# Performance work log

Hardware: AMD Instinct MI355X
Metric: run time of the kernel (lower is better)

The kernel has to match this reference:

```python
import jax, jax.numpy as jnp
import numpy as np

B, TOKEN_DIM, HIDDEN_DIM, K = 32768, 1024, 512, 8192


def setup_inputs() -> dict:
    key = jax.random.key(0)
    k1, k2, k3 = jax.random.split(key, 3)
    tokens = jax.random.normal(k1, (B, TOKEN_DIM), dtype=jnp.float32)
    # nn.Linear weight init in the module: randn * 0.1, bias zero
    W = jax.random.normal(k2, (HIDDEN_DIM, TOKEN_DIM), dtype=jnp.float32) * 0.1
    b = jnp.zeros((HIDDEN_DIM,), dtype=jnp.float32)
    codebook = jax.random.normal(k3, (K, HIDDEN_DIM), dtype=jnp.float32)
    return {"tokens": tokens, "W": W, "b": b, "codebook": codebook}


def reference(tokens, W, b, codebook):
    # 1. Linear projection: [B, token_dim] -> [B, hidden_dim]
    h = tokens @ W.T + b
    # 2. Pairwise Euclidean distances to codebook: [B, K]
    #    ||h - c||^2 = ||h||^2 + ||c||^2 - 2 h.c  (clamped for numerical safety)
    h_sq = jnp.sum(h * h, axis=-1, keepdims=True)            # [B, 1]
    c_sq = jnp.sum(codebook * codebook, axis=-1)              # [K]
    d2 = h_sq + c_sq[None, :] - 2.0 * (h @ codebook.T)        # [B, K]
    dist = jnp.sqrt(jnp.maximum(d2, 0.0))
    # 3. Hard nearest-codebook lookup
    return jnp.argmin(dist, axis=-1).astype(jnp.int64)
```

## Files before the change

kernel.cpp:

```cpp
#include <hip/hip_runtime.h>
#include <stdint.h>

typedef __attribute__((ext_vector_type(8))) _Float16 f16x8;
typedef __attribute__((ext_vector_type(4))) float f32x4;

namespace {
constexpr int NB = 32768;
constexpr int TD = 1024;
constexpr int HD = 512;
constexpr int KC = 8192;

constexpr size_t WS_H      = 0;
constexpr size_t WS_CHF    = WS_H + (size_t)NB * HD * 4;
constexpr size_t WS_CSQ32  = WS_CHF + (size_t)KC * HD * 2;
constexpr size_t WS_PART   = WS_CSQ32 + (size_t)KC * 4;
constexpr size_t WS_NEED   = WS_PART + (size_t)NB * 16 * 8;
constexpr size_t WS_H16    = WS_NEED;
constexpr size_t WS_NEED2  = WS_H16 + (size_t)NB * HD * 2;
}

__device__ __forceinline__ void g2lds16(const void* g, void* l) {
    __builtin_amdgcn_global_load_lds(
        (const __attribute__((address_space(1))) void*)g,
        (__attribute__((address_space(3))) void*)l, 16, 0, 0);
}

__global__ void k0_prep_cb(const float* __restrict__ cb, uint8_t* __restrict__ ws) {
    _Float16* chf = (_Float16*)(ws + WS_CHF);
    const int wv = threadIdx.x >> 6, lane = threadIdx.x & 63;
    const int row = blockIdx.x * 4 + wv;
    const size_t base = (size_t)row * HD + lane * 8;
    const float4 a = *(const float4*)&cb[base];
    const float4 b = *(const float4*)&cb[base + 4];
    const float cf[8] = {a.x, a.y, a.z, a.w, b.x, b.y, b.z, b.w};
    f16x8 hv;
    #pragma unroll
    for (int e = 0; e < 8; ++e) hv[e] = (_Float16)cf[e];
    *(f16x8*)&chf[base] = hv;
}

__global__ void k0_csq(const float* __restrict__ cb, uint8_t* __restrict__ ws) {
    float* csq32 = (float*)(ws + WS_CSQ32);
    const int code = blockIdx.x * 256 + threadIdx.x;
    const float* crow = &cb[(size_t)code * HD];
    float sq = 0.0f;
    #pragma unroll 4
    for (int kq = 0; kq < HD / 4; ++kq) {
        const float4 v = *(const float4*)&crow[kq * 4];
        sq = fmaf(v.x, v.x, sq);
        sq = fmaf(v.y, v.y, sq);
        sq = fmaf(v.z, v.z, sq);
        sq = fmaf(v.w, v.w, sq);
    }
    csq32[code] = sq;
}

template<bool H16>
__launch_bounds__(256, 2)
__global__ void k1_hgemm(const float* __restrict__ tokens,
                         const float* __restrict__ W,
                         const float* __restrict__ bias,
                         uint8_t* __restrict__ ws) {
    __shared__ __align__(16) float Tt[32][132];
    __shared__ __align__(16) float Wt[32][132];
    float* h = (float*)(ws + WS_H);
    _Float16* h16 = (_Float16*)(ws + WS_H16);

    const int tid = threadIdx.x;
    const int rows0 = blockIdx.x * 128;
    const int hcol0 = blockIdx.y * 128;
    const int rx = tid & 15;
    const int cx = tid >> 4;
    const int srow = tid >> 1;
    const int shalf = tid & 1;

    float acc[8][8];
    #pragma unroll
    for (int i = 0; i < 8; ++i)
        #pragma unroll
        for (int j = 0; j < 8; ++j) acc[i][j] = 0.0f;

    #pragma unroll 1
    for (int kt = 0; kt < TD; kt += 32) {
        __syncthreads();
        {
            const float* tsrc = &tokens[(size_t)(rows0 + srow) * TD + kt + shalf * 16];
            const float* wsrc = &W[(size_t)(hcol0 + srow) * TD + kt + shalf * 16];
            #pragma unroll
            for (int q = 0; q < 4; ++q) {
                const float4 tv = *(const float4*)&tsrc[q * 4];
                const float4 wv = *(const float4*)&wsrc[q * 4];
                const int k0 = shalf * 16 + q * 4;
                Tt[k0 + 0][srow] = tv.x; Tt[k0 + 1][srow] = tv.y;
                Tt[k0 + 2][srow] = tv.z; Tt[k0 + 3][srow] = tv.w;
                Wt[k0 + 0][srow] = wv.x; Wt[k0 + 1][srow] = wv.y;
                Wt[k0 + 2][srow] = wv.z; Wt[k0 + 3][srow] = wv.w;
            }
        }
        __syncthreads();
        #pragma unroll 2
        for (int kk = 0; kk < 32; ++kk) {
            const float4 a0 = *(const float4*)&Tt[kk][rx * 8];
            const float4 a1 = *(const float4*)&Tt[kk][rx * 8 + 4];
            const float4 b0 = *(const float4*)&Wt[kk][cx * 8];
            const float4 b1 = *(const float4*)&Wt[kk][cx * 8 + 4];
            const float av[8] = {a0.x, a0.y, a0.z, a0.w, a1.x, a1.y, a1.z, a1.w};
            const float bv[8] = {b0.x, b0.y, b0.z, b0.w, b1.x, b1.y, b1.z, b1.w};
            #pragma unroll
            for (int i = 0; i < 8; ++i)
                #pragma unroll
                for (int j = 0; j < 8; ++j)
                    acc[i][j] = fmaf(av[i], bv[j], acc[i][j]);
        }
    }

    float bj[8];
    #pragma unroll
    for (int j = 0; j < 8; ++j) bj[j] = bias[hcol0 + cx * 8 + j];
    #pragma unroll
    for (int i = 0; i < 8; ++i) {
        const int row = rows0 + rx * 8 + i;
        float o[8];
        #pragma unroll
        for (int j = 0; j < 8; ++j) o[j] = acc[i][j] + bj[j];
        float4 o0, o1;
        o0.x = o[0]; o0.y = o[1]; o0.z = o[2]; o0.w = o[3];
        o1.x = o[4]; o1.y = o[5]; o1.z = o[6]; o1.w = o[7];
        *(float4*)&h[(size_t)row * HD + hcol0 + cx * 8] = o0;
        *(float4*)&h[(size_t)row * HD + hcol0 + cx * 8 + 4] = o1;
        if constexpr (H16) {
            f16x8 hv;
            #pragma unroll
            for (int j = 0; j < 8; ++j) hv[j] = (_Float16)o[j];
            *(f16x8*)&h16[(size_t)row * HD + hcol0 + cx * 8] = hv;
        }
    }
}

template<bool H16>
__launch_bounds__(256, 2)
__global__ void k2_score(uint8_t* __restrict__ ws) {
    __shared__ __align__(16) _Float16 At[128 * 32], Bt[128 * 32];
    __shared__ unsigned long long dump[128][16];
    const float* h = (const float*)(ws + WS_H);
    const _Float16* h16 = (const _Float16*)(ws + WS_H16);
    const _Float16* chf = (const _Float16*)(ws + WS_CHF);
    const float* csq32 = (const float*)(ws + WS_CSQ32);
    unsigned long long* part = (unsigned long long*)(ws + WS_PART);

    const int tid = threadIdx.x;
    const int l = tid & 63;
    const int w = tid >> 6;
    const int wr = w >> 1, wc = w & 1;
    const int rows0 = blockIdx.x * 128;
    const int codes0 = blockIdx.y * 2048;

    unsigned long long cand0[16], cand1[16];
    #pragma unroll
    for (int s = 0; s < 16; ++s) { cand0[s] = ~0ull; cand1[s] = ~0ull; }

    #pragma unroll 1
    for (int cc = 0; cc < 16; ++cc) {
        const int codebase = codes0 + cc * 128;
        f32x4 acc[4][4];
        #pragma unroll
        for (int m = 0; m < 4; ++m)
            #pragma unroll
            for (int n = 0; n < 4; ++n) acc[m][n] = (f32x4)(0.0f);

        #pragma unroll 1
        for (int kt = 0; kt < HD; kt += 32) {
            __syncthreads();
            if constexpr (H16) {
                #pragma unroll
                for (int i = 0; i < 2; ++i) {
                    const int sub = w * 2 + i;
                    const int arow = sub * 16 + (l >> 2);
                    g2lds16(h16 + (size_t)(rows0 + arow) * HD + kt + (l & 3) * 8,
                            At + sub * 512);
                    const int crow = sub * 16 + (l >> 2);
                    g2lds16(chf + (size_t)(codebase + crow) * HD + kt + (l & 3) * 8,
                            Bt + sub * 512);
                }
            } else {
                #pragma unroll
                for (int i = 0; i < 2; ++i) {
                    const int sub = w * 2 + i;
                    const int crow = sub * 16 + (l >> 2);
                    g2lds16(chf + (size_t)(codebase + crow) * HD + kt + (l & 3) * 8,
                            Bt + sub * 512);
                }
                const int arow = tid >> 1, ahalf = tid & 1;
                const float* hsrc = &h[(size_t)(rows0 + arow) * HD + kt + ahalf * 16];
                const float4 q0 = *(const float4*)&hsrc[0];
                const float4 q1 = *(const float4*)&hsrc[4];
                const float4 q2 = *(const float4*)&hsrc[8];
                const float4 q3 = *(const float4*)&hsrc[12];
                f16x8 v0, v1;
                v0[0] = (_Float16)q0.x; v0[1] = (_Float16)q0.y;
                v0[2] = (_Float16)q0.z; v0[3] = (_Float16)q0.w;
                v0[4] = (_Float16)q1.x; v0[5] = (_Float16)q1.y;
                v0[6] = (_Float16)q1.z; v0[7] = (_Float16)q1.w;
                v1[0] = (_Float16)q2.x; v1[1] = (_Float16)q2.y;
                v1[2] = (_Float16)q2.z; v1[3] = (_Float16)q2.w;
                v1[4] = (_Float16)q3.x; v1[5] = (_Float16)q3.y;
                v1[6] = (_Float16)q3.z; v1[7] = (_Float16)q3.w;
                *(f16x8*)&At[arow * 32 + ahalf * 16] = v0;
                *(f16x8*)&At[arow * 32 + ahalf * 16 + 8] = v1;
            }
            __syncthreads();
            f16x8 af[4], bfr[4];
            #pragma unroll
            for (int m = 0; m < 4; ++m)
                af[m] = *(const f16x8*)&At[(wr * 64 + m * 16 + (l & 15)) * 32 + (l >> 4) * 8];
            #pragma unroll
            for (int n = 0; n < 4; ++n)
                bfr[n] = *(const f16x8*)&Bt[(wc * 64 + n * 16 + (l & 15)) * 32 + (l >> 4) * 8];
            #pragma unroll
            for (int m = 0; m < 4; ++m)
                #pragma unroll
                for (int n = 0; n < 4; ++n)
                    acc[m][n] = __builtin_amdgcn_mfma_f32_16x16x32_f16(af[m], bfr[n], acc[m][n], 0, 0, 0);
        }

        #pragma unroll
        for (int n = 0; n < 4; ++n) {
            const int code = codebase + wc * 64 + n * 16 + (l & 15);
            const float cs = csq32[code];
            #pragma unroll
            for (int m = 0; m < 4; ++m)
                #pragma unroll
                for (int reg = 0; reg < 4; ++reg) {
                    const float s = fmaf(-2.0f, acc[m][n][reg], cs);
                    const uint32_t b = __float_as_uint(s);
                    const uint32_t msk = (uint32_t)((int32_t)b >> 31);
                    const uint32_t key = b ^ (msk | 0x80000000u);
                    const unsigned long long k64 =
                        ((unsigned long long)key << 32) | (unsigned long long)(uint32_t)code;
                    const int slot = m * 4 + reg;
                    if (k64 < cand0[slot]) { cand1[slot] = cand0[slot]; cand0[slot] = k64; }
                    else if (k64 < cand1[slot]) { cand1[slot] = k64; }
                }
        }
    }

    #pragma unroll
    for (int m = 0; m < 4; ++m)
        #pragma unroll
        for (int reg = 0; reg < 4; ++reg) {
            const int slot = m * 4 + reg;
            unsigned long long c0 = cand0[slot], c1 = cand1[slot];
            #pragma unroll
            for (int mask = 1; mask < 4; mask <<= 1) {
                const unsigned long long o0 = __shfl_xor(c0, mask, 64);
                const unsigned long long o1 = __shfl_xor(c1, mask, 64);
                if (o0 < c0) { c1 = (c0 < o1) ? c0 : o1; c0 = o0; }
                else         { c1 = (c1 < o0) ? c1 : o0; }
            }
            if ((l & 3) == 0) {
                const int rloc = wr * 64 + m * 16 + (l >> 4) * 4 + reg;
                const int g = (l >> 2) & 3;
                dump[rloc][wc * 8 + g * 2 + 0] = c0;
                dump[rloc][wc * 8 + g * 2 + 1] = c1;
            }
        }
    __syncthreads();

    if (tid < 128) {
        unsigned long long t0 = ~0ull, t1 = ~0ull, t2 = ~0ull, t3 = ~0ull;
        #pragma unroll 1
        for (int e = 0; e < 16; ++e) {
            const unsigned long long v = dump[tid][e];
            if (v < t0)      { t3 = t2; t2 = t1; t1 = t0; t0 = v; }
            else if (v < t1) { t3 = t2; t2 = t1; t1 = v; }
            else if (v < t2) { t3 = t2; t2 = v; }
            else if (v < t3) { t3 = v; }
        }
        const size_t pbase = (size_t)(rows0 + tid) * 16 + blockIdx.y * 4;
        part[pbase + 0] = t0;
        part[pbase + 1] = t1;
        part[pbase + 2] = t2;
        part[pbase + 3] = t3;
    }
}

__launch_bounds__(256, 4)
__global__ void k3_rescore(const float* __restrict__ codebook,
                           const uint8_t* __restrict__ ws,
                           int* __restrict__ out) {
    const float* h = (const float*)(ws + WS_H);
    const float* csq32 = (const float*)(ws + WS_CSQ32);
    const unsigned long long* part = (const unsigned long long*)(ws + WS_PART);
    __shared__ unsigned long long red[16][16];

    const int tid = threadIdx.x;
    const int rloc = tid >> 4;
    const int slot = tid & 15;
    const int row = blockIdx.x * 16 + rloc;

    const int idx = (int)(uint32_t)(part[(size_t)row * 16 + slot] & 0xFFFFFFFFull);
    const float* hrow = &h[(size_t)row * HD];
    const float* crow = &codebook[(size_t)idx * HD];

    float hc = 0.0f;
    #pragma unroll 4
    for (int kq = 0; kq < HD / 4; ++kq) {
        const float4 hv = *(const float4*)&hrow[kq * 4];
        const float4 cv = *(const float4*)&crow[kq * 4];
        hc = fmaf(hv.x, cv.x, hc);
        hc = fmaf(hv.y, cv.y, hc);
        hc = fmaf(hv.z, cv.z, hc);
        hc = fmaf(hv.w, cv.w, hc);
    }
    const float s = fmaf(-2.0f, hc, csq32[idx]);

    const uint32_t b = __float_as_uint(s);
    const uint32_t key = (b & 0x80000000u) ? ~b : (b | 0x80000000u);
    red[rloc][slot] = ((unsigned long long)key << 32) | (unsigned long long)(uint32_t)idx;
    __syncthreads();

    if (tid < 16) {
        unsigned long long m = red[tid][0];
        #pragma unroll
        for (int e = 1; e < 16; ++e) {
            const unsigned long long v = red[tid][e];
            if (v < m) m = v;
        }
        out[blockIdx.x * 16 + tid] = (int)(uint32_t)(m & 0xFFFFFFFFull);
    }
}

__launch_bounds__(256, 1)
__global__ void qenc_fallback(const float* __restrict__ tokens,
                              const float* __restrict__ W,
                              const float* __restrict__ bias,
                              const float* __restrict__ codebook,
                              int* __restrict__ out)
{
    __shared__ __align__(16) float h_t[HD][64];
    __shared__ __align__(16) float stage[32 * 256];
    const int tid = threadIdx.x;
    const int rowbase = blockIdx.x * 64;
    {
        const int tx = tid & 15, ty = tid >> 4, sr = tid >> 2, sq = tid & 3;
        float* Wt = stage;
        float* Tt = stage + 32 * 64;
        #pragma unroll 1
        for (int hb = 0; hb < HD; hb += 64) {
            float acc[4][4];
            #pragma unroll
            for (int i = 0; i < 4; ++i)
                #pragma unroll
                for (int j = 0; j < 4; ++j) acc[i][j] = 0.0f;
            #pragma unroll 1
            for (int kt = 0; kt < TD; kt += 32) {
                __syncthreads();
                const float4 w0 = *(const float4*)&W[(hb + sr) * TD + kt + sq * 8];
                const float4 w1 = *(const float4*)&W[(hb + sr) * TD + kt + sq * 8 + 4];
                const float4 t0 = *(const float4*)&tokens[(rowbase + sr) * TD + kt + sq * 8];
                const float4 t1 = *(const float4*)&tokens[(rowbase + sr) * TD + kt + sq * 8 + 4];
                Wt[(sq * 8 + 0) * 64 + sr] = w0.x; Wt[(sq * 8 + 1) * 64 + sr] = w0.y;
                Wt[(sq * 8 + 2) * 64 + sr] = w0.z; Wt[(sq * 8 + 3) * 64 + sr] = w0.w;
                Wt[(sq * 8 + 4) * 64 + sr] = w1.x; Wt[(sq * 8 + 5) * 64 + sr] = w1.y;
                Wt[(sq * 8 + 6) * 64 + sr] = w1.z; Wt[(sq * 8 + 7) * 64 + sr] = w1.w;
                Tt[(sq * 8 + 0) * 64 + sr] = t0.x; Tt[(sq * 8 + 1) * 64 + sr] = t0.y;
                Tt[(sq * 8 + 2) * 64 + sr] = t0.z; Tt[(sq * 8 + 3) * 64 + sr] = t0.w;
                Tt[(sq * 8 + 4) * 64 + sr] = t1.x; Tt[(sq * 8 + 5) * 64 + sr] = t1.y;
                Tt[(sq * 8 + 6) * 64 + sr] = t1.z; Tt[(sq * 8 + 7) * 64 + sr] = t1.w;
                __syncthreads();
                #pragma unroll 8
                for (int kk = 0; kk < 32; ++kk) {
                    const float4 wv = *(const float4*)&Wt[kk * 64 + ty * 4];
                    const float4 tv = *(const float4*)&Tt[kk * 64 + tx * 4];
                    const float wf[4] = {wv.x, wv.y, wv.z, wv.w};
                    const float tf[4] = {tv.x, tv.y, tv.z, tv.w};
                    #pragma unroll
                    for (int i = 0; i < 4; ++i)
                        #pragma unroll
                        for (int j = 0; j < 4; ++j)
                            acc[i][j] = fmaf(wf[i], tf[j], acc[i][j]);
                }
            }
            #pragma unroll
            for (int i = 0; i < 4; ++i) {
                const float bb = bias[hb + ty * 4 + i];
                float4 o; o.x = acc[i][0] + bb; o.y = acc[i][1] + bb;
                o.z = acc[i][2] + bb; o.w = acc[i][3] + bb;
                *(float4*)&h_t[hb + ty * 4 + i][tx * 4] = o;
            }
        }
    }
    __syncthreads();
    {
        const int tx = tid & 31, ty = tid >> 5, sc = tid >> 3, sf = tid & 7;
        float bv[2][4]; int bi[2][4];
        #pragma unroll
        for (int ii = 0; ii < 2; ++ii)
            #pragma unroll
            for (int i = 0; i < 4; ++i) { bv[ii][i] = 3.4e38f; bi[ii][i] = 0; }
        #pragma unroll 1
        for (int cbase = 0; cbase < KC; cbase += 256) {
            float acc[2][2][4][4];
            #pragma unroll
            for (int ii = 0; ii < 2; ++ii)
                #pragma unroll
                for (int jj = 0; jj < 2; ++jj)
                    #pragma unroll
                    for (int i = 0; i < 4; ++i)
                        #pragma unroll
                        for (int j = 0; j < 4; ++j) acc[ii][jj][i][j] = 0.0f;
            float csqv = 0.0f;
            #pragma unroll 1
            for (int kt = 0; kt < HD; kt += 32) {
                __syncthreads();
                #pragma unroll
                for (int cg = 0; cg < 8; ++cg) {
                    const int c = cg * 32 + sc;
                    const float4 v = *(const float4*)&codebook[(cbase + c) * HD + kt + sf * 4];
                    stage[(sf * 4 + 0) * 256 + c] = v.x;
                    stage[(sf * 4 + 1) * 256 + c] = v.y;
                    stage[(sf * 4 + 2) * 256 + c] = v.z;
                    stage[(sf * 4 + 3) * 256 + c] = v.w;
                }
                __syncthreads();
                #pragma unroll 8
                for (int kk = 0; kk < 32; ++kk) {
                    const float v = stage[kk * 256 + tid];
                    csqv = fmaf(v, v, csqv);
                }
                #pragma unroll 4
                for (int kk = 0; kk < 32; ++kk) {
                    const float4 h0 = *(const float4*)&h_t[kt + kk][ty * 4];
                    const float4 h1 = *(const float4*)&h_t[kt + kk][ty * 4 + 32];
                    const float4 c0 = *(const float4*)&stage[kk * 256 + tx * 4];
                    const float4 c1 = *(const float4*)&stage[kk * 256 + 128 + tx * 4];
                    const float ha[2][4] = {{h0.x, h0.y, h0.z, h0.w}, {h1.x, h1.y, h1.z, h1.w}};
                    const float cf2[2][4] = {{c0.x, c0.y, c0.z, c0.w}, {c1.x, c1.y, c1.z, c1.w}};
                    #pragma unroll
                    for (int ii = 0; ii < 2; ++ii)
                        #pragma unroll
                        for (int jj = 0; jj < 2; ++jj)
                            #pragma unroll
                            for (int i = 0; i < 4; ++i)
                                #pragma unroll
                                for (int j = 0; j < 4; ++j)
                                    acc[ii][jj][i][j] = fmaf(ha[ii][i], cf2[jj][j], acc[ii][jj][i][j]);
                }
            }
            __syncthreads();
            stage[tid] = csqv;
            __syncthreads();
            #pragma unroll
            for (int jj = 0; jj < 2; ++jj)
                #pragma unroll
                for (int j = 0; j < 4; ++j) {
                    const int cloc = jj * 128 + tx * 4 + j;
                    const float cs = stage[cloc];
                    const int code = cbase + cloc;
                    #pragma unroll
                    for (int ii = 0; ii < 2; ++ii)
                        #pragma unroll
                        for (int i = 0; i < 4; ++i) {
                            const float s = fmaf(-2.0f, acc[ii][jj][i][j], cs);
                            if (s < bv[ii][i] || (s == bv[ii][i] && code < bi[ii][i])) {
                                bv[ii][i] = s; bi[ii][i] = code;
                            }
                        }
                }
        }
        #pragma unroll
        for (int ii = 0; ii < 2; ++ii)
            #pragma unroll
            for (int i = 0; i < 4; ++i) {
                float v = bv[ii][i]; int idx = bi[ii][i];
                #pragma unroll
                for (int m = 1; m < 32; m <<= 1) {
                    const float ov = __shfl_xor(v, m, 64);
                    const int   oi = __shfl_xor(idx, m, 64);
                    if (ov < v || (ov == v && oi < idx)) { v = ov; idx = oi; }
                }
                if (tx == 0) out[rowbase + ii * 32 + ty * 4 + i] = idx;
            }
    }
}

extern "C" void kernel_launch(void* const* d_in, const int* in_sizes, int n_in,
                              void* d_out, int out_size, void* d_ws, size_t ws_size,
                              hipStream_t stream) {
    const float* tokens   = (const float*)d_in[0];
    const float* W        = (const float*)d_in[1];
    const float* bias     = (const float*)d_in[2];
    const float* codebook = (const float*)d_in[3];
    int* out = (int*)d_out;
    uint8_t* ws = (uint8_t*)d_ws;

    if (ws_size < WS_NEED) {
        qenc_fallback<<<NB / 64, 256, 0, stream>>>(tokens, W, bias, codebook, out);
        return;
    }
    k0_prep_cb<<<KC / 4, 256, 0, stream>>>(codebook, ws);
    k0_csq<<<KC / 256, 256, 0, stream>>>(codebook, ws);
    if (ws_size >= WS_NEED2) {
        k1_hgemm<true><<<dim3(NB / 128, HD / 128), 256, 0, stream>>>(tokens, W, bias, ws);
        k2_score<true><<<dim3(NB / 128, KC / 2048), 256, 0, stream>>>(ws);
    } else {
        k1_hgemm<false><<<dim3(NB / 128, HD / 128), 256, 0, stream>>>(tokens, W, bias, ws);
        k2_score<false><<<dim3(NB / 128, KC / 2048), 256, 0, stream>>>(ws);
    }
    k3_rescore<<<NB / 16, 256, 0, stream>>>(codebook, ws, out);
}
```

Before: 994.6 us.

## Double-buffer LDS tiles in score kernel to overlap loads with MFMA

The score kernel now keeps two LDS buffers for each of the A and B tiles. The next k-slice, or the first slice of the next code chunk, is staged into the other buffer before the current tile's MFMAs run, so each k-step needs one barrier instead of two. The intent is to hide global-to-LDS load latency behind matrix math. The candidate dump area now reuses the A buffer after a final barrier, which keeps total LDS usage about the same as before.

```diff
diff --git a/kernel.cpp b/kernel.cpp
--- a/kernel.cpp
+++ b/kernel.cpp
@@ -140,8 +140,8 @@
 template<bool H16>
 __launch_bounds__(256, 2)
 __global__ void k2_score(uint8_t* __restrict__ ws) {
-    __shared__ __align__(16) _Float16 At[128 * 32], Bt[128 * 32];
-    __shared__ unsigned long long dump[128][16];
+    __shared__ __align__(16) _Float16 At[2 * 8 * 512];
+    __shared__ __align__(16) _Float16 Bt[2 * 8 * 512];
     const float* h = (const float*)(ws + WS_H);
     const _Float16* h16 = (const _Float16*)(ws + WS_H16);
     const _Float16* chf = (const _Float16*)(ws + WS_CHF);
@@ -159,6 +159,47 @@
     #pragma unroll
     for (int s = 0; s < 16; ++s) { cand0[s] = ~0ull; cand1[s] = ~0ull; }
 
+    auto stage = [&](int buf, int codebase, int kt) {
+        if constexpr (H16) {
+            #pragma unroll
+            for (int i = 0; i < 2; ++i) {
+                const int sub = w * 2 + i;
+                const int r = sub * 16 + (l >> 2);
+                g2lds16(h16 + (size_t)(rows0 + r) * HD + kt + (l & 3) * 8,
+                        At + buf * 4096 + sub * 512);
+                g2lds16(chf + (size_t)(codebase + r) * HD + kt + (l & 3) * 8,
+                        Bt + buf * 4096 + sub * 512);
+            }
+        } else {
+            #pragma unroll
+            for (int i = 0; i < 2; ++i) {
+                const int sub = w * 2 + i;
+                const int r = sub * 16 + (l >> 2);
+                g2lds16(chf + (size_t)(codebase + r) * HD + kt + (l & 3) * 8,
+                        Bt + buf * 4096 + sub * 512);
+            }
+            const int arow = tid >> 1, ahalf = tid & 1;
+            const float* hsrc = &h[(size_t)(rows0 + arow) * HD + kt + ahalf * 16];
+            const float4 q0 = *(const float4*)&hsrc[0];
+            const float4 q1 = *(const float4*)&hsrc[4];
+            const float4 q2 = *(const float4*)&hsrc[8];
+            const float4 q3 = *(const float4*)&hsrc[12];
+            f16x8 v0, v1;
+            v0[0] = (_Float16)q0.x; v0[1] = (_Float16)q0.y;
+            v0[2] = (_Float16)q0.z; v0[3] = (_Float16)q0.w;
+            v0[4] = (_Float16)q1.x; v0[5] = (_Float16)q1.y;
+            v0[6] = (_Float16)q1.z; v0[7] = (_Float16)q1.w;
+            v1[0] = (_Float16)q2.x; v1[1] = (_Float16)q2.y;
+            v1[2] = (_Float16)q2.z; v1[3] = (_Float16)q2.w;
+            v1[4] = (_Float16)q3.x; v1[5] = (_Float16)q3.y;
+            v1[6] = (_Float16)q3.z; v1[7] = (_Float16)q3.w;
+            *(f16x8*)&At[buf * 4096 + arow * 32 + ahalf * 16] = v0;
+            *(f16x8*)&At[buf * 4096 + arow * 32 + ahalf * 16 + 8] = v1;
+        }
+    };
+
+    stage(0, codes0, 0);
+
     #pragma unroll 1
     for (int cc = 0; cc < 16; ++cc) {
         const int codebase = codes0 + cc * 128;
@@ -168,54 +209,22 @@
             #pragma unroll
             for (int n = 0; n < 4; ++n) acc[m][n] = (f32x4)(0.0f);
 
-        #pragma unroll 1
-        for (int kt = 0; kt < HD; kt += 32) {
+        #pragma unroll 2
+        for (int kt16 = 0; kt16 < 16; ++kt16) {
+            const int cur = kt16 & 1;
             __syncthreads();
-            if constexpr (H16) {
-                #pragma unroll
-                for (int i = 0; i < 2; ++i) {
-                    const int sub = w * 2 + i;
-                    const int arow = sub * 16 + (l >> 2);
-                    g2lds16(h16 + (size_t)(rows0 + arow) * HD + kt + (l & 3) * 8,
-                            At + sub * 512);
-                    const int crow = sub * 16 + (l >> 2);
-                    g2lds16(chf + (size_t)(codebase + crow) * HD + kt + (l & 3) * 8,
-                            Bt + sub * 512);
-                }
-            } else {
-                #pragma unroll
-                for (int i = 0; i < 2; ++i) {
-                    const int sub = w * 2 + i;
-                    const int crow = sub * 16 + (l >> 2);
-                    g2lds16(chf + (size_t)(codebase + crow) * HD + kt + (l & 3) * 8,
-                            Bt + sub * 512);
-                }
-                const int arow = tid >> 1, ahalf = tid & 1;
-                const float* hsrc = &h[(size_t)(rows0 + arow) * HD + kt + ahalf * 16];
-                const float4 q0 = *(const float4*)&hsrc[0];
-                const float4 q1 = *(const float4*)&hsrc[4];
-                const float4 q2 = *(const float4*)&hsrc[8];
-                const float4 q3 = *(const float4*)&hsrc[12];
-                f16x8 v0, v1;
-                v0[0] = (_Float16)q0.x; v0[1] = (_Float16)q0.y;
-                v0[2] = (_Float16)q0.z; v0[3] = (_Float16)q0.w;
-                v0[4] = (_Float16)q1.x; v0[5] = (_Float16)q1.y;
-                v0[6] = (_Float16)q1.z; v0[7] = (_Float16)q1.w;
-                v1[0] = (_Float16)q2.x; v1[1] = (_Float16)q2.y;
-                v1[2] = (_Float16)q2.z; v1[3] = (_Float16)q2.w;
-                v1[4] = (_Float16)q3.x; v1[5] = (_Float16)q3.y;
-                v1[6] = (_Float16)q3.z; v1[7] = (_Float16)q3.w;
-                *(f16x8*)&At[arow * 32 + ahalf * 16] = v0;
-                *(f16x8*)&At[arow * 32 + ahalf * 16 + 8] = v1;
-            }
-            __syncthreads();
+            if (!(cc == 15 && kt16 == 15)) {
+                const int ncc = (kt16 == 15) ? cc + 1 : cc;
+                const int nkt = (kt16 == 15) ? 0 : kt16 + 1;
+                stage(cur ^ 1, codes0 + ncc * 128, nkt * 32);
+            }
             f16x8 af[4], bfr[4];
             #pragma unroll
             for (int m = 0; m < 4; ++m)
-                af[m] = *(const f16x8*)&At[(wr * 64 + m * 16 + (l & 15)) * 32 + (l >> 4) * 8];
+                af[m] = *(const f16x8*)&At[cur * 4096 + (wr * 64 + m * 16 + (l & 15)) * 32 + (l >> 4) * 8];
             #pragma unroll
             for (int n = 0; n < 4; ++n)
-                bfr[n] = *(const f16x8*)&Bt[(wc * 64 + n * 16 + (l & 15)) * 32 + (l >> 4) * 8];
+                bfr[n] = *(const f16x8*)&Bt[cur * 4096 + (wc * 64 + n * 16 + (l & 15)) * 32 + (l >> 4) * 8];
             #pragma unroll
             for (int m = 0; m < 4; ++m)
                 #pragma unroll
@@ -243,6 +252,9 @@
                 }
         }
     }
+
+    __syncthreads();
+    unsigned long long (*dump)[16] = (unsigned long long (*)[16])At;
 
     #pragma unroll
     for (int m = 0; m < 4; ++m)
```

After: 1.053 ms. 1.06x slower.

## Double K-tile depth to 64 with XOR-swizzled LDS layout in score kernel

Applied to the files above, without the earlier changes.

The score GEMM's K step per LDS tile grows from 32 to 64, halving the number of barrier pairs per code chunk. The LDS rows are XOR-swizzled by row index to avoid bank conflicts on the wider 128-byte rows. The separate dump buffer is removed and aliased onto At after a barrier, so total LDS stays within the occupancy budget of two blocks per CU. The trade-off is larger staging per iteration and some extra index arithmetic.

```diff
diff --git a/kernel.cpp b/kernel.cpp
--- a/kernel.cpp
+++ b/kernel.cpp
@@ -140,8 +140,8 @@
 template<bool H16>
 __launch_bounds__(256, 2)
 __global__ void k2_score(uint8_t* __restrict__ ws) {
-    __shared__ __align__(16) _Float16 At[128 * 32], Bt[128 * 32];
-    __shared__ unsigned long long dump[128][16];
+    __shared__ __align__(16) _Float16 At[128 * 64];
+    __shared__ __align__(16) _Float16 Bt[128 * 64];
     const float* h = (const float*)(ws + WS_H);
     const _Float16* h16 = (const _Float16*)(ws + WS_H16);
     const _Float16* chf = (const _Float16*)(ws + WS_CHF);
@@ -155,6 +155,9 @@
     const int rows0 = blockIdx.x * 128;
     const int codes0 = blockIdx.y * 2048;
 
+    const int sr = l >> 3;
+    const int scnk = (l & 7) ^ sr;
+
     unsigned long long cand0[16], cand1[16];
     #pragma unroll
     for (int s = 0; s < 16; ++s) { cand0[s] = ~0ull; cand1[s] = ~0ull; }
@@ -169,58 +172,56 @@
             for (int n = 0; n < 4; ++n) acc[m][n] = (f32x4)(0.0f);
 
         #pragma unroll 1
-        for (int kt = 0; kt < HD; kt += 32) {
+        for (int kt = 0; kt < HD; kt += 64) {
             __syncthreads();
+            #pragma unroll
+            for (int i = 0; i < 4; ++i) {
+                const int sub = w * 4 + i;
+                g2lds16(chf + (size_t)(codebase + sub * 8 + sr) * HD + kt + scnk * 8,
+                        Bt + sub * 512);
+            }
             if constexpr (H16) {
                 #pragma unroll
-                for (int i = 0; i < 2; ++i) {
-                    const int sub = w * 2 + i;
-                    const int arow = sub * 16 + (l >> 2);
-                    g2lds16(h16 + (size_t)(rows0 + arow) * HD + kt + (l & 3) * 8,
+                for (int i = 0; i < 4; ++i) {
+                    const int sub = w * 4 + i;
+                    g2lds16(h16 + (size_t)(rows0 + sub * 8 + sr) * HD + kt + scnk * 8,
                             At + sub * 512);
-                    const int crow = sub * 16 + (l >> 2);
-                    g2lds16(chf + (size_t)(codebase + crow) * HD + kt + (l & 3) * 8,
-                            Bt + sub * 512);
                 }
             } else {
-                #pragma unroll
-                for (int i = 0; i < 2; ++i) {
-                    const int sub = w * 2 + i;
-                    const int crow = sub * 16 + (l >> 2);
-                    g2lds16(chf + (size_t)(codebase + crow) * HD + kt + (l & 3) * 8,
-                            Bt + sub * 512);
-                }
                 const int arow = tid >> 1, ahalf = tid & 1;
-                const float* hsrc = &h[(size_t)(rows0 + arow) * HD + kt + ahalf * 16];
-                const float4 q0 = *(const float4*)&hsrc[0];
-                const float4 q1 = *(const float4*)&hsrc[4];
-                const float4 q2 = *(const float4*)&hsrc[8];
-                const float4 q3 = *(const float4*)&hsrc[12];
-                f16x8 v0, v1;
-                v0[0] = (_Float16)q0.x; v0[1] = (_Float16)q0.y;
-                v0[2] = (_Float16)q0.z; v0[3] = (_Float16)q0.w;
-                v0[4] = (_Float16)q1.x; v0[5] = (_Float16)q1.y;
-                v0[6] = (_Float16)q1.z; v0[7] = (_Float16)q1.w;
-                v1[0] = (_Float16)q2.x; v1[1] = (_Float16)q2.y;
-                v1[2] = (_Float16)q2.z; v1[3] = (_Float16)q2.w;
-                v1[4] = (_Float16)q3.x; v1[5] = (_Float16)q3.y;
-                v1[6] = (_Float16)q3.z; v1[7] = (_Float16)q3.w;
-                *(f16x8*)&At[arow * 32 + ahalf * 16] = v0;
-                *(f16x8*)&At[arow * 32 + ahalf * 16 + 8] = v1;
+                const float* hsrc = &h[(size_t)(rows0 + arow) * HD + kt + ahalf * 32];
+                #pragma unroll
+                for (int j = 0; j < 4; ++j) {
+                    const float4 q0 = *(const float4*)&hsrc[j * 8];
+                    const float4 q1 = *(const float4*)&hsrc[j * 8 + 4];
+                    f16x8 v;
+                    v[0] = (_Float16)q0.x; v[1] = (_Float16)q0.y;
+                    v[2] = (_Float16)q0.z; v[3] = (_Float16)q0.w;
+                    v[4] = (_Float16)q1.x; v[5] = (_Float16)q1.y;
+                    v[6] = (_Float16)q1.z; v[7] = (_Float16)q1.w;
+                    const int cs = (ahalf * 4 + j) ^ (arow & 7);
+                    *(f16x8*)&At[arow * 64 + cs * 8] = v;
+                }
             }
             __syncthreads();
-            f16x8 af[4], bfr[4];
-            #pragma unroll
-            for (int m = 0; m < 4; ++m)
-                af[m] = *(const f16x8*)&At[(wr * 64 + m * 16 + (l & 15)) * 32 + (l >> 4) * 8];
-            #pragma unroll
-            for (int n = 0; n < 4; ++n)
-                bfr[n] = *(const f16x8*)&Bt[(wc * 64 + n * 16 + (l & 15)) * 32 + (l >> 4) * 8];
-            #pragma unroll
-            for (int m = 0; m < 4; ++m)
+
+            #pragma unroll
+            for (int s = 0; s < 2; ++s) {
+                f16x8 af[4], bfr[4];
+                #pragma unroll
+                for (int m = 0; m < 4; ++m)
+                    af[m] = *(const f16x8*)&At[(wr * 64 + m * 16 + (l & 15)) * 64 +
+                                               (((s * 4 + (l >> 4)) ^ (l & 7)) * 8)];
                 #pragma unroll
                 for (int n = 0; n < 4; ++n)
-                    acc[m][n] = __builtin_amdgcn_mfma_f32_16x16x32_f16(af[m], bfr[n], acc[m][n], 0, 0, 0);
+                    bfr[n] = *(const f16x8*)&Bt[(wc * 64 + n * 16 + (l & 15)) * 64 +
+                                                (((s * 4 + (l >> 4)) ^ (l & 7)) * 8)];
+                #pragma unroll
+                for (int m = 0; m < 4; ++m)
+                    #pragma unroll
+                    for (int n = 0; n < 4; ++n)
+                        acc[m][n] = __builtin_amdgcn_mfma_f32_16x16x32_f16(af[m], bfr[n], acc[m][n], 0, 0, 0);
+            }
         }
 
         #pragma unroll
@@ -243,6 +244,9 @@
                 }
         }
     }
+
+    __syncthreads();
+    unsigned long long (*dump)[16] = (unsigned long long (*)[16])At;
 
     #pragma unroll
     for (int m = 0; m < 4; ++m)
```

Measured after the change: 928.4 us. 6.7% less time.
